# Performance work log

Hardware: AMD Instinct MI355X
Metric: run time of the kernel (lower is better)

The kernel has to match this reference:

```python
import jax, jax.numpy as jnp
import numpy as np
import math

B, L, D, H, DEPTH = 2, 1024, 1024, 16, 4
INNER = int(D * 4 * 2 / 3)  # 2730
HD = D // H
SCALE = D ** 0.5


def _get_slopes(n):
    def pow2(n):
        start = 2 ** (-2 ** (-(math.log2(n) - 3)))
        return [start * start ** i for i in range(n)]
    if math.log2(n).is_integer():
        return pow2(n)
    c = 2 ** math.floor(math.log2(n))
    return pow2(c) + _get_slopes(2 * c)[0::2][: n - c]


def setup_inputs() -> dict:
    key = jax.random.key(0)
    ks = jax.random.split(key, 8)
    def rn(k, shape, s=0.02):
        return jax.random.normal(k, shape, dtype=jnp.float32) * s
    return {
        "x": jax.random.normal(ks[0], (B, L, D), dtype=jnp.float32),
        "slopes": jnp.asarray(np.asarray(_get_slopes(H), dtype=np.float32).reshape(H, 1, 1)),
        "gamma_attn": jnp.ones((DEPTH, D), jnp.float32),
        "in_proj_w": rn(ks[1], (DEPTH, 3 * D, D)),
        "in_proj_b": jnp.zeros((DEPTH, 3 * D), jnp.float32),
        "out_proj_w": rn(ks[2], (DEPTH, D, D)),
        "out_proj_b": jnp.zeros((DEPTH, D), jnp.float32),
        "gamma_ff": jnp.ones((DEPTH, D), jnp.float32),
        "ff_w1": rn(ks[3], (DEPTH, 2 * INNER, D)),
        "ff_b1": jnp.zeros((DEPTH, 2 * INNER), jnp.float32),
        "ff_w2": rn(ks[4], (DEPTH, D, INNER)),
        "ff_b2": jnp.zeros((DEPTH, D), jnp.float32),
        "final_gamma": jnp.ones((D,), jnp.float32),
    }


def _rmsnorm(t, gamma):
    # F.normalize(x, dim=-1) * sqrt(dim) * gamma
    n = jnp.linalg.norm(t, axis=-1, keepdims=True)
    return t / jnp.maximum(n, 1e-12) * SCALE * gamma


def reference(x, slopes, gamma_attn, in_proj_w, in_proj_b, out_proj_w, out_proj_b,
              gamma_ff, ff_w1, ff_b1, ff_w2, ff_b2, final_gamma):
    Bsz, Ls, Dm = x.shape
    pos = jnp.arange(Ls)
    # ALiBi bias: -(|i-j|) * per-head slope -> (H, L, L); shared across batch
    alibi = (-jnp.abs(pos[None, :] - pos[:, None]).astype(jnp.float32))[None] * slopes
    for i in range(DEPTH):
        # attention block
        a_in = _rmsnorm(x, gamma_attn[i])
        qkv = a_in @ in_proj_w[i].T + in_proj_b[i]  # (B, L, 3D)
        q, k, v = jnp.split(qkv, 3, axis=-1)
        q = q.reshape(Bsz, Ls, H, HD).transpose(0, 2, 1, 3)
        k = k.reshape(Bsz, Ls, H, HD).transpose(0, 2, 1, 3)
        v = v.reshape(Bsz, Ls, H, HD).transpose(0, 2, 1, 3)
        scores = jnp.einsum('bhqd,bhkd->bhqk', q, k) / math.sqrt(HD) + alibi[None]
        attn = jax.nn.softmax(scores, axis=-1)
        o = jnp.einsum('bhqk,bhkd->bhqd', attn, v).transpose(0, 2, 1, 3).reshape(Bsz, Ls, Dm)
        x = o @ out_proj_w[i].T + out_proj_b[i] + x
        # GEGLU feed-forward block
        f_in = _rmsnorm(x, gamma_ff[i])
        h = f_in @ ff_w1[i].T + ff_b1[i]
        a, gate = jnp.split(h, 2, axis=-1)
        x = (jax.nn.gelu(gate, approximate=False) * a) @ ff_w2[i].T + ff_b2[i] + x
    return _rmsnorm(x, final_gamma)
```

## Files before the change

### kernel.cpp

```cpp
#include <hip/hip_runtime.h>

#define DEPTH   4
#define BSZ     2
#define LSEQ    1024
#define DMODEL  1024
#define NHEAD   16
#define HDIM    64
#define MROWS   (BSZ*LSEQ)
#define INNER   2730
#define INNERP  2752
#define N1      (2*INNER)
#define N1P     (2*INNERP)
#define LOG2E   1.4426950408889634f
#define NSPLIT  2

typedef __bf16 bf16;
typedef bf16  bf16x8 __attribute__((ext_vector_type(8)));
typedef float f32x4  __attribute__((ext_vector_type(4)));
typedef uint32_t u32x4 __attribute__((ext_vector_type(4)));

__device__ inline f32x4 mfma16(bf16x8 a, bf16x8 b, f32x4 c) {
  return __builtin_amdgcn_mfma_f32_16x16x32_bf16(a, b, c, 0, 0, 0);
}

__device__ inline void gload_lds16(const void* g, void* l) {
  __builtin_amdgcn_global_load_lds(
      (const __attribute__((address_space(1))) void*)g,
      (__attribute__((address_space(3))) void*)l, 16, 0, 0);
}

__global__ void conv_bf16_kernel(const float* __restrict__ src, bf16* __restrict__ dst, size_t n) {
  size_t i = ((size_t)blockIdx.x * 256 + threadIdx.x) * 8;
  if (i >= n) return;
  float4 v0 = *(const float4*)(src + i);
  float4 v1 = *(const float4*)(src + i + 4);
  bf16x8 o = { (bf16)v0.x,(bf16)v0.y,(bf16)v0.z,(bf16)v0.w,
               (bf16)v1.x,(bf16)v1.y,(bf16)v1.z,(bf16)v1.w };
  *(bf16x8*)(dst + i) = o;
}

__global__ void conv_w1_kernel(const float* __restrict__ src, bf16* __restrict__ dst) {
  size_t i = ((size_t)blockIdx.x * 256 + threadIdx.x) * 8;
  const size_t tot = (size_t)DEPTH * N1P * DMODEL;
  if (i >= tot) return;
  int d  = (int)(i / ((size_t)N1P * DMODEL));
  int rem = (int)(i % ((size_t)N1P * DMODEL));
  int rp = rem / DMODEL, k = rem % DMODEL;
  int p2 = rp >> 4, w = rp & 15;
  int col = ((p2 >> 1) << 4) + w;
  bf16x8 o;
  if (col >= INNER) {
    o = (bf16x8)(bf16)0.f;
  } else {
    int rs = (p2 & 1) ? (INNER + col) : col;
    const float* s = src + ((size_t)d * N1 + rs) * DMODEL + k;
    float4 v0 = *(const float4*)s;
    float4 v1 = *(const float4*)(s + 4);
    o = bf16x8{ (bf16)v0.x,(bf16)v0.y,(bf16)v0.z,(bf16)v0.w,
                (bf16)v1.x,(bf16)v1.y,(bf16)v1.z,(bf16)v1.w };
  }
  *(bf16x8*)(dst + i) = o;
}

__global__ void conv_b1_kernel(const float* __restrict__ src, float* __restrict__ dst) {
  int i = blockIdx.x * 256 + threadIdx.x;
  if (i >= DEPTH * N1P) return;
  int d = i / N1P, rp = i % N1P;
  int p2 = rp >> 4, w = rp & 15;
  int col = ((p2 >> 1) << 4) + w;
  float v = 0.f;
  if (col < INNER) v = src[d * N1 + ((p2 & 1) ? (INNER + col) : col)];
  dst[i] = v;
}

__global__ void conv_w2_kernel(const float* __restrict__ src, bf16* __restrict__ dst) {
  size_t i = ((size_t)blockIdx.x * 256 + threadIdx.x) * 8;
  const size_t tot = (size_t)DEPTH * DMODEL * INNERP;
  if (i >= tot) return;
  size_t dn = i / INNERP;
  int kp = (int)(i % INNERP);
  const float* s = src + dn * INNER;
  bf16x8 o;
  #pragma unroll
  for (int j = 0; j < 8; ++j) {
    int k = kp + j;
    o[j] = (k < INNER) ? (bf16)s[k] : (bf16)0.f;
  }
  *(bf16x8*)(dst + i) = o;
}

template<bool OUT_BF16>
__global__ __launch_bounds__(256) void rmsnorm_kernel(const float* __restrict__ x,
    const float* __restrict__ gamma, void* __restrict__ out) {
  const int row = blockIdx.x;
  const int tid = threadIdx.x;
  const float4 v = *(const float4*)(x + (size_t)row * DMODEL + tid * 4);
  float ss = v.x*v.x + v.y*v.y + v.z*v.z + v.w*v.w;
  for (int m = 1; m < 64; m <<= 1) ss += __shfl_xor(ss, m);
  __shared__ float ws4[4];
  if ((tid & 63) == 0) ws4[tid >> 6] = ss;
  __syncthreads();
  float tot = ws4[0] + ws4[1] + ws4[2] + ws4[3];
  float scale = 32.0f / fmaxf(sqrtf(tot), 1e-12f);
  const float4 g = *(const float4*)(gamma + tid * 4);
  float o0 = v.x*scale*g.x, o1 = v.y*scale*g.y, o2 = v.z*scale*g.z, o3 = v.w*scale*g.w;
  size_t p = (size_t)row * DMODEL + tid * 4;
  if (OUT_BF16) {
    bf16* ob = (bf16*)out;
    ob[p+0] = (bf16)o0; ob[p+1] = (bf16)o1; ob[p+2] = (bf16)o2; ob[p+3] = (bf16)o3;
  } else {
    *(float4*)((float*)out + p) = make_float4(o0, o1, o2, o3);
  }
}

template<int TN, int EPI, bool CHUNK_M>
__global__ __launch_bounds__(256) void gemm_bt(const bf16* __restrict__ A,
    const bf16* __restrict__ Bw, const float* __restrict__ bias,
    void* __restrict__ Cout, int M_, int N_, int Kstr, int nk0, int nkTot) {
  constexpr int NFR = TN / 32;
  constexpr int BCH = TN / 32;
  __shared__ __attribute__((aligned(16))) bf16 As[2][128 * 64];
  __shared__ __attribute__((aligned(16))) bf16 Bs[2][TN * 64];
  const int tid  = threadIdx.x;
  const int lane = tid & 63;
  const int wid  = tid >> 6;
  const int wr = wid >> 1, wc = wid & 1;

  const int z = blockIdx.z;
  const int nk  = z ? (nkTot - nk0) : nk0;
  const int kOff = z * (nk0 << 6);

  const int gx = gridDim.x, gy = gridDim.y;
  const int nwg = gx * gy;
  int bid = blockIdx.y * gx + blockIdx.x;
  int swz = bid;
  if ((nwg & 7) == 0) swz = (bid & 7) * (nwg >> 3) + (bid >> 3);
  int mIdx, nIdx;
  if (CHUNK_M) { nIdx = swz % gx; mIdx = swz / gx; }
  else         { mIdx = swz % gy; nIdx = swz / gy; }
  const int m0 = mIdx * 128;
  const int n0 = nIdx * TN;

  const int q = lane & 15, G = lane >> 4;
  const int s7 = q & 7;
  const int srow = tid >> 3;
  const int scol = ((tid & 7) ^ (srow & 7)) << 3;

  f32x4 acc[4][NFR] = {};

  auto stage = [&](int buf, int kt) {
    const int k0 = kOff + (kt << 6);
    #pragma unroll
    for (int j = 0; j < 4; ++j) {
      gload_lds16(A + (size_t)(m0 + j*32 + srow) * Kstr + k0 + scol,
                  &As[buf][(j * 256 + wid * 64) << 3]);
    }
    #pragma unroll
    for (int j = 0; j < BCH; ++j) {
      gload_lds16(Bw + (size_t)(n0 + j*32 + srow) * Kstr + k0 + scol,
                  &Bs[buf][(j * 256 + wid * 64) << 3]);
    }
  };

  stage(0, 0);
  asm volatile("s_waitcnt vmcnt(0)" ::: "memory");
  __syncthreads();

  int cur = 0;
  for (int kt = 0; kt < nk; ++kt) {
    if (kt + 1 < nk) stage(cur ^ 1, kt + 1);
    #pragma unroll
    for (int kk = 0; kk < 2; ++kk) {
      const int c0 = kk * 4 + G;
      bf16x8 af[4], bfr[NFR];
      #pragma unroll
      for (int m = 0; m < 4; ++m)
        af[m] = *(const bf16x8*)(&As[cur][(wr*64 + m*16 + q) * 64 + ((c0 ^ s7) << 3)]);
      #pragma unroll
      for (int n = 0; n < NFR; ++n)
        bfr[n] = *(const bf16x8*)(&Bs[cur][(wc*(TN/2) + n*16 + q) * 64 + ((c0 ^ s7) << 3)]);
      #pragma unroll
      for (int m = 0; m < 4; ++m)
        #pragma unroll
        for (int n = 0; n < NFR; ++n)
          acc[m][n] = mfma16(af[m], bfr[n], acc[m][n]);
    }
    asm volatile("s_waitcnt vmcnt(0)" ::: "memory");
    __syncthreads();
    cur ^= 1;
  }

  const int rb = G << 2;
  const int cl = q;
  if (EPI == 2) {
    #pragma unroll
    for (int m = 0; m < 4; ++m) {
      #pragma unroll
      for (int np = 0; np < NFR/2; ++np) {
        int ca = n0 + wc*(TN/2) + (2*np)*16 + cl;
        int cg = ca + 16;
        float ba = bias[ca], bg = bias[cg];
        int colo = ((ca >> 5) << 4) + cl;
        #pragma unroll
        for (int r = 0; r < 4; ++r) {
          int row = m0 + wr*64 + m*16 + rb + r;
          float av = acc[m][2*np][r] + ba;
          float gv = acc[m][2*np+1][r] + bg;
          float gl = 0.5f * gv * (1.f + erff(gv * 0.70710678118654752f));
          ((bf16*)Cout)[(size_t)row * (N_ >> 1) + colo] = (bf16)(av * gl);
        }
      }
    }
  } else if (EPI == 3) {
    #pragma unroll
    for (int m = 0; m < 4; ++m) {
      #pragma unroll
      for (int n = 0; n < NFR; ++n) {
        int col = n0 + wc*(TN/2) + n*16 + cl;
        float bv = (z == 0) ? bias[col] : 0.f;
        #pragma unroll
        for (int r = 0; r < 4; ++r) {
          int row = m0 + wr*64 + m*16 + rb + r;
          atomicAdd((float*)Cout + (size_t)row * N_ + col, acc[m][n][r] + bv);
        }
      }
    }
  } else {
    #pragma unroll
    for (int m = 0; m < 4; ++m) {
      #pragma unroll
      for (int n = 0; n < NFR; ++n) {
        int col = n0 + wc*(TN/2) + n*16 + cl;
        float bv = bias[col];
        #pragma unroll
        for (int r = 0; r < 4; ++r) {
          int row = m0 + wr*64 + m*16 + rb + r;
          ((bf16*)Cout)[(size_t)row * N_ + col] = (bf16)(acc[m][n][r] + bv);
        }
      }
    }
  }
}

__global__ __launch_bounds__(256) void attn_kernel(const bf16* __restrict__ qkv,
    const float* __restrict__ slopes, float* __restrict__ Opart, float* __restrict__ ml) {
  const int tid = threadIdx.x, lane = tid & 63, wid = tid >> 6;
  const int bh = blockIdx.y;
  const int b = bh >> 4, h = bh & 15;
  const int kvz = blockIdx.z;
  const int kv0 = kvz * (LSEQ / NSPLIT);
  const float slope2 = slopes[h] * LOG2E;
  const float SC = 0.125f * LOG2E;
  const int qw = blockIdx.x * 64 + wid * 16;

  __shared__ __attribute__((aligned(16))) bf16     Kt[64 * 72];
  __shared__ __attribute__((aligned(16))) uint32_t V32[64 * 36];
  __shared__ __attribute__((aligned(16))) uint32_t Pl32[4][16 * 36];

  const size_t rs = 3 * DMODEL;
  const size_t base = (size_t)b * LSEQ * rs;

  bf16x8 qf[2];
  {
    const bf16* p = qkv + base + (size_t)(qw + (lane & 15)) * rs + h * HDIM + ((lane >> 4) << 3);
    qf[0] = *(const bf16x8*)p;
    qf[1] = *(const bf16x8*)(p + 32);
  }

  f32x4 accO[4] = {};
  float mrow[4], lrow[4];
  #pragma unroll
  for (int r = 0; r < 4; ++r) { mrow[r] = -1e30f; lrow[r] = 0.f; }

  const int trow = tid >> 2;
  const int tcol = (tid & 3) << 4;

  bf16x8 kreg0, kreg1, vreg0, vreg1;
  {
    const bf16* kp = qkv + base + (size_t)(kv0 + trow) * rs + DMODEL + h * HDIM + tcol;
    kreg0 = *(const bf16x8*)kp; kreg1 = *(const bf16x8*)(kp + 8);
    const bf16* vp = qkv + base + (size_t)(kv0 + trow) * rs + 2 * DMODEL + h * HDIM + tcol;
    vreg0 = *(const bf16x8*)vp; vreg1 = *(const bf16x8*)(vp + 8);
  }

  uint32_t* P32w = &Pl32[wid][0];
  const int q = lane & 15, G = lane >> 4;

  for (int kv = kv0; kv < kv0 + LSEQ / NSPLIT; kv += 64) {
    __syncthreads();
    *(bf16x8*)(Kt + trow * 72 + tcol)     = kreg0;
    *(bf16x8*)(Kt + trow * 72 + tcol + 8) = kreg1;
    {
      u32x4 va = __builtin_bit_cast(u32x4, vreg0);
      u32x4 vb = __builtin_bit_cast(u32x4, vreg1);
      u32x4 pa, pb;
      #pragma unroll
      for (int i = 0; i < 4; ++i) {
        pa[i] = (uint32_t)__shfl_xor((int)va[i], 4);
        pb[i] = (uint32_t)__shfl_xor((int)vb[i], 4);
      }
      const bool oddk = (trow & 1);
      const int d0 = tcol + (oddk ? 8 : 0);
      u32x4 m = oddk ? vb : va;
      u32x4 oo = oddk ? pb : pa;
      const int kpair = trow >> 1;
      const int swz = kpair ^ ((d0 >> 3) << 1);
      #pragma unroll
      for (int i = 0; i < 4; ++i) {
        uint32_t lo = oddk ? oo[i] : m[i];
        uint32_t hi = oddk ? m[i] : oo[i];
        uint32_t w0 = (lo & 0xffffu) | (hi << 16);
        uint32_t w1 = (lo >> 16) | (hi & 0xffff0000u);
        V32[(d0 + 2*i)     * 36 + swz] = w0;
        V32[(d0 + 2*i + 1) * 36 + swz] = w1;
      }
    }
    __syncthreads();

    if (kv + 64 < kv0 + LSEQ / NSPLIT) {
      const bf16* kp = qkv + base + (size_t)(kv + 64 + trow) * rs + DMODEL + h * HDIM + tcol;
      kreg0 = *(const bf16x8*)kp; kreg1 = *(const bf16x8*)(kp + 8);
      const bf16* vp = qkv + base + (size_t)(kv + 64 + trow) * rs + 2 * DMODEL + h * HDIM + tcol;
      vreg0 = *(const bf16x8*)vp; vreg1 = *(const bf16x8*)(vp + 8);
    }

    f32x4 sacc[4] = {};
    __builtin_amdgcn_s_setprio(1);
    #pragma unroll
    for (int nt = 0; nt < 4; ++nt) {
      const bf16* kb = Kt + (nt * 16 + q) * 72 + (G << 3);
      sacc[nt] = mfma16(qf[0], *(const bf16x8*)kb, sacc[nt]);
      sacc[nt] = mfma16(qf[1], *(const bf16x8*)(kb + 32), sacc[nt]);
    }
    __builtin_amdgcn_s_setprio(0);

    float pv[4][4];
    #pragma unroll
    for (int r = 0; r < 4; ++r) {
      int qi = qw + (G << 2) + r;
      float vmax = -1e30f;
      #pragma unroll
      for (int nt = 0; nt < 4; ++nt) {
        int kj = kv + nt * 16 + q;
        float s = sacc[nt][r] * SC - slope2 * fabsf((float)(qi - kj));
        pv[nt][r] = s;
        vmax = fmaxf(vmax, s);
      }
      for (int m = 1; m < 16; m <<= 1) vmax = fmaxf(vmax, __shfl_xor(vmax, m));
      float newmax = fmaxf(mrow[r], vmax);
      float ef = exp2f(mrow[r] - newmax);
      float rsum = 0.f;
      #pragma unroll
      for (int nt = 0; nt < 4; ++nt) {
        float p = exp2f(pv[nt][r] - newmax);
        pv[nt][r] = p;
        rsum += p;
      }
      for (int m = 1; m < 16; m <<= 1) rsum += __shfl_xor(rsum, m);
      lrow[r] = lrow[r] * ef + rsum;
      mrow[r] = newmax;
      #pragma unroll
      for (int dn = 0; dn < 4; ++dn) accO[dn][r] *= ef;
    }

    #pragma unroll
    for (int nt = 0; nt < 4; ++nt) {
      #pragma unroll
      for (int r = 0; r < 4; ++r) {
        float other = __shfl_xor(pv[nt][r], 1);
        if (!(lane & 1)) {
          uint32_t w;
          asm("v_cvt_pk_bf16_f32 %0, %1, %2" : "=v"(w) : "v"(pv[nt][r]), "v"(other));
          int prow = (G << 2) + r;
          int col2 = nt * 8 + (q >> 1);
          P32w[prow * 36 + (col2 ^ ((prow & 7) << 1))] = w;
        }
      }
    }
    asm volatile("s_waitcnt lgkmcnt(0)" ::: "memory");

    __builtin_amdgcn_s_setprio(1);
    #pragma unroll
    for (int chunk = 0; chunk < 2; ++chunk) {
      u32x4 praw = *(const u32x4*)(P32w + q * 36 + chunk * 16 + 4 * (G ^ ((q >> 1) & 3)));
      if (q & 1) praw = __builtin_shufflevector(praw, praw, 2, 3, 0, 1);
      bf16x8 pf = __builtin_bit_cast(bf16x8, praw);
      #pragma unroll
      for (int dn = 0; dn < 4; ++dn) {
        const int d = dn * 16 + q;
        u32x4 raw = *(const u32x4*)(V32 + d * 36 + chunk * 16 + 4 * (G ^ dn));
        if ((lane >> 3) & 1) raw = __builtin_shufflevector(raw, raw, 2, 3, 0, 1);
        bf16x8 vf = __builtin_bit_cast(bf16x8, raw);
        accO[dn] = mfma16(pf, vf, accO[dn]);
      }
    }
    __builtin_amdgcn_s_setprio(0);
  }

  #pragma unroll
  for (int r = 0; r < 4; ++r) {
    int qr = qw + (G << 2) + r;
    size_t obase = ((size_t)(kvz * 32 + bh) * LSEQ + qr) * HDIM;
    #pragma unroll
    for (int dn = 0; dn < 4; ++dn)
      Opart[obase + dn * 16 + q] = accO[dn][r];
    if (q == 0) {
      size_t mb = ((size_t)(kvz * 32 + bh) * LSEQ + qr) * 2;
      ml[mb]     = mrow[r];
      ml[mb + 1] = lrow[r];
    }
  }
}

__global__ __launch_bounds__(256) void attn_combine(const float* __restrict__ Opart,
    const float* __restrict__ ml, bf16* __restrict__ o) {
  int idx = blockIdx.x * 256 + threadIdx.x;
  int bh = idx >> 14;
  int rem = idx & 16383;
  int qr = rem >> 4;
  int d4 = (rem & 15) << 2;
  float mz[NSPLIT], lz[NSPLIT];
  float m = -1e30f;
  #pragma unroll
  for (int z = 0; z < NSPLIT; ++z) {
    size_t rz = ((size_t)(z * 32 + bh) * LSEQ + qr) * 2;
    mz[z] = ml[rz]; lz[z] = ml[rz + 1];
    m = fmaxf(m, mz[z]);
  }
  float wz[NSPLIT];
  float l = 0.f;
  #pragma unroll
  for (int z = 0; z < NSPLIT; ++z) { wz[z] = exp2f(mz[z] - m); l += lz[z] * wz[z]; }
  float inv = 1.f / l;
  float ax = 0, ay = 0, az = 0, aw = 0;
  #pragma unroll
  for (int z = 0; z < NSPLIT; ++z) {
    size_t rz = (size_t)(z * 32 + bh) * LSEQ + qr;
    float4 ov = *(const float4*)(Opart + rz * HDIM + d4);
    ax += ov.x * wz[z]; ay += ov.y * wz[z]; az += ov.z * wz[z]; aw += ov.w * wz[z];
  }
  int b = bh >> 4, h = bh & 15;
  bf16* op = o + ((size_t)(b * LSEQ + qr) * DMODEL + h * HDIM + d4);
  op[0] = (bf16)(ax * inv);
  op[1] = (bf16)(ay * inv);
  op[2] = (bf16)(az * inv);
  op[3] = (bf16)(aw * inv);
}

extern "C" void kernel_launch(void* const* d_in, const int* in_sizes, int n_in,
                              void* d_out, int out_size, void* d_ws, size_t ws_size,
                              hipStream_t stream) {
  const float* x_in      = (const float*)d_in[0];
  const float* slopes    = (const float*)d_in[1];
  const float* g_attn    = (const float*)d_in[2];
  const float* w_in      = (const float*)d_in[3];
  const float* b_in      = (const float*)d_in[4];
  const float* w_out     = (const float*)d_in[5];
  const float* b_out     = (const float*)d_in[6];
  const float* g_ff      = (const float*)d_in[7];
  const float* w1        = (const float*)d_in[8];
  const float* b1        = (const float*)d_in[9];
  const float* w2        = (const float*)d_in[10];
  const float* b2        = (const float*)d_in[11];
  const float* g_final   = (const float*)d_in[12];

  char* p = (char*)d_ws;
  float* xw   = (float*)p;              p += (size_t)MROWS * DMODEL * 4;
  bf16* abuf  = (bf16*)p;               p += (size_t)MROWS * DMODEL * 2;
  bf16* qkvb  = (bf16*)p;               p += (size_t)MROWS * 3 * DMODEL * 2;
  bf16* obuf  = (bf16*)p;               p += (size_t)MROWS * DMODEL * 2;
  bf16* gbuf  = (bf16*)p;               p += (size_t)MROWS * INNERP * 2;
  float* Opart = (float*)p;             p += (size_t)NSPLIT * 32 * LSEQ * HDIM * 4;
  float* mlb   = (float*)p;             p += (size_t)NSPLIT * 32 * LSEQ * 2 * 4;
  bf16* w_in_b  = (bf16*)p;             p += (size_t)DEPTH * 3 * DMODEL * DMODEL * 2;
  bf16* w_out_b = (bf16*)p;             p += (size_t)DEPTH * DMODEL * DMODEL * 2;
  bf16* w1p     = (bf16*)p;             p += (size_t)DEPTH * N1P * DMODEL * 2;
  bf16* w2p     = (bf16*)p;             p += (size_t)DEPTH * DMODEL * INNERP * 2;
  float* b1p    = (float*)p;            p += (size_t)DEPTH * N1P * 4;

  hipMemcpyAsync(xw, x_in, (size_t)MROWS * DMODEL * 4, hipMemcpyDeviceToDevice, stream);

  conv_bf16_kernel<<<6144, 256, 0, stream>>>(w_in, w_in_b, (size_t)DEPTH * 3 * DMODEL * DMODEL);
  conv_bf16_kernel<<<2048, 256, 0, stream>>>(w_out, w_out_b, (size_t)DEPTH * DMODEL * DMODEL);
  conv_w1_kernel<<<11008, 256, 0, stream>>>(w1, w1p);
  conv_b1_kernel<<<86, 256, 0, stream>>>(b1, b1p);
  conv_w2_kernel<<<5504, 256, 0, stream>>>(w2, w2p);

  for (int i = 0; i < DEPTH; ++i) {
    rmsnorm_kernel<true><<<MROWS, 256, 0, stream>>>(xw, g_attn + i * DMODEL, abuf);
    gemm_bt<64, 0, false><<<dim3(48, 16), 256, 0, stream>>>(
        abuf, w_in_b + (size_t)i * 3 * DMODEL * DMODEL, b_in + i * 3 * DMODEL,
        qkvb, MROWS, 3 * DMODEL, DMODEL, 16, 16);
    attn_kernel<<<dim3(16, 32, NSPLIT), 256, 0, stream>>>(qkvb, slopes, Opart, mlb);
    attn_combine<<<2048, 256, 0, stream>>>(Opart, mlb, obuf);
    gemm_bt<64, 3, true><<<dim3(16, 16, 2), 256, 0, stream>>>(
        obuf, w_out_b + (size_t)i * DMODEL * DMODEL, b_out + i * DMODEL,
        xw, MROWS, DMODEL, DMODEL, 8, 16);
    rmsnorm_kernel<true><<<MROWS, 256, 0, stream>>>(xw, g_ff + i * DMODEL, abuf);
    gemm_bt<64, 2, false><<<dim3(86, 16), 256, 0, stream>>>(
        abuf, w1p + (size_t)i * N1P * DMODEL, b1p + i * N1P,
        gbuf, MROWS, N1P, DMODEL, 16, 16);
    gemm_bt<64, 3, true><<<dim3(16, 16, 2), 256, 0, stream>>>(
        gbuf, w2p + (size_t)i * DMODEL * INNERP, b2 + i * DMODEL,
        xw, MROWS, DMODEL, INNERP, 22, 43);
  }
  rmsnorm_kernel<false><<<MROWS, 256, 0, stream>>>(xw, g_final, d_out);
}
```

Measured before the change: 794.5 us.

## Transpose QK^T MFMA in attention to keep softmax rows lane-local, skip LDS for P

```diff
diff --git a/kernel.cpp b/kernel.cpp
--- a/kernel.cpp
+++ b/kernel.cpp
@@ -255,22 +255,21 @@
 
   __shared__ __attribute__((aligned(16))) bf16     Kt[64 * 72];
   __shared__ __attribute__((aligned(16))) uint32_t V32[64 * 36];
-  __shared__ __attribute__((aligned(16))) uint32_t Pl32[4][16 * 36];
 
   const size_t rs = 3 * DMODEL;
   const size_t base = (size_t)b * LSEQ * rs;
+  const int q = lane & 15, G = lane >> 4;
+  const float qi = (float)(qw + q);
 
   bf16x8 qf[2];
   {
-    const bf16* p = qkv + base + (size_t)(qw + (lane & 15)) * rs + h * HDIM + ((lane >> 4) << 3);
+    const bf16* p = qkv + base + (size_t)(qw + q) * rs + h * HDIM + (G << 3);
     qf[0] = *(const bf16x8*)p;
     qf[1] = *(const bf16x8*)(p + 32);
   }
 
   f32x4 accO[4] = {};
-  float mrow[4], lrow[4];
-  #pragma unroll
-  for (int r = 0; r < 4; ++r) { mrow[r] = -1e30f; lrow[r] = 0.f; }
+  float mreg = -1e30f, lreg = 0.f;
 
   const int trow = tid >> 2;
   const int tcol = (tid & 3) << 4;
@@ -282,9 +281,6 @@
     const bf16* vp = qkv + base + (size_t)(kv0 + trow) * rs + 2 * DMODEL + h * HDIM + tcol;
     vreg0 = *(const bf16x8*)vp; vreg1 = *(const bf16x8*)(vp + 8);
   }
-
-  uint32_t* P32w = &Pl32[wid][0];
-  const int q = lane & 15, G = lane >> 4;
 
   for (int kv = kv0; kv < kv0 + LSEQ / NSPLIT; kv += 64) {
     __syncthreads();
@@ -329,62 +325,75 @@
     #pragma unroll
     for (int nt = 0; nt < 4; ++nt) {
       const bf16* kb = Kt + (nt * 16 + q) * 72 + (G << 3);
-      sacc[nt] = mfma16(qf[0], *(const bf16x8*)kb, sacc[nt]);
-      sacc[nt] = mfma16(qf[1], *(const bf16x8*)(kb + 32), sacc[nt]);
+      sacc[nt] = mfma16(*(const bf16x8*)kb, qf[0], sacc[nt]);
+      sacc[nt] = mfma16(*(const bf16x8*)(kb + 32), qf[1], sacc[nt]);
     }
     __builtin_amdgcn_s_setprio(0);
 
     float pv[4][4];
-    #pragma unroll
-    for (int r = 0; r < 4; ++r) {
-      int qi = qw + (G << 2) + r;
-      float vmax = -1e30f;
-      #pragma unroll
-      for (int nt = 0; nt < 4; ++nt) {
-        int kj = kv + nt * 16 + q;
-        float s = sacc[nt][r] * SC - slope2 * fabsf((float)(qi - kj));
+    float pmax = -1e30f;
+    #pragma unroll
+    for (int nt = 0; nt < 4; ++nt) {
+      #pragma unroll
+      for (int r = 0; r < 4; ++r) {
+        float kj = (float)(kv + nt * 16 + (G << 2) + r);
+        float s = sacc[nt][r] * SC - slope2 * fabsf(qi - kj);
         pv[nt][r] = s;
-        vmax = fmaxf(vmax, s);
-      }
-      for (int m = 1; m < 16; m <<= 1) vmax = fmaxf(vmax, __shfl_xor(vmax, m));
-      float newmax = fmaxf(mrow[r], vmax);
-      float ef = exp2f(mrow[r] - newmax);
-      float rsum = 0.f;
-      #pragma unroll
-      for (int nt = 0; nt < 4; ++nt) {
-        float p = exp2f(pv[nt][r] - newmax);
-        pv[nt][r] = p;
-        rsum += p;
-      }
-      for (int m = 1; m < 16; m <<= 1) rsum += __shfl_xor(rsum, m);
-      lrow[r] = lrow[r] * ef + rsum;
-      mrow[r] = newmax;
-      #pragma unroll
-      for (int dn = 0; dn < 4; ++dn) accO[dn][r] *= ef;
-    }
-
+        pmax = fmaxf(pmax, s);
+      }
+    }
+    pmax = fmaxf(pmax, __shfl_xor(pmax, 16));
+    pmax = fmaxf(pmax, __shfl_xor(pmax, 32));
+
+    if (!__all(pmax <= mreg + 8.f)) {
+      float mnew = fmaxf(mreg, pmax);
+      float ef = exp2f(mreg - mnew);
+      mreg = mnew;
+      lreg *= ef;
+      float efr[4];
+      #pragma unroll
+      for (int r = 0; r < 4; ++r)
+        efr[r] = __shfl(ef, (G << 4) + (G << 2) + r);
+      #pragma unroll
+      for (int dn = 0; dn < 4; ++dn)
+        #pragma unroll
+        for (int r = 0; r < 4; ++r)
+          accO[dn][r] *= efr[r];
+    }
+
+    float rsum = 0.f;
     #pragma unroll
     for (int nt = 0; nt < 4; ++nt) {
       #pragma unroll
       for (int r = 0; r < 4; ++r) {
-        float other = __shfl_xor(pv[nt][r], 1);
-        if (!(lane & 1)) {
-          uint32_t w;
-          asm("v_cvt_pk_bf16_f32 %0, %1, %2" : "=v"(w) : "v"(pv[nt][r]), "v"(other));
-          int prow = (G << 2) + r;
-          int col2 = nt * 8 + (q >> 1);
-          P32w[prow * 36 + (col2 ^ ((prow & 7) << 1))] = w;
-        }
-      }
-    }
-    asm volatile("s_waitcnt lgkmcnt(0)" ::: "memory");
+        float pe = exp2f(pv[nt][r] - mreg);
+        pv[nt][r] = pe;
+        rsum += pe;
+      }
+    }
+    rsum += __shfl_xor(rsum, 16);
+    rsum += __shfl_xor(rsum, 32);
+    lreg += rsum;
+
+    uint32_t wp[4][2];
+    #pragma unroll
+    for (int nt = 0; nt < 4; ++nt) {
+      asm("v_cvt_pk_bf16_f32 %0, %1, %2" : "=v"(wp[nt][0]) : "v"(pv[nt][0]), "v"(pv[nt][1]));
+      asm("v_cvt_pk_bf16_f32 %0, %1, %2" : "=v"(wp[nt][1]) : "v"(pv[nt][2]), "v"(pv[nt][3]));
+    }
 
     __builtin_amdgcn_s_setprio(1);
     #pragma unroll
     for (int chunk = 0; chunk < 2; ++chunk) {
-      u32x4 praw = *(const u32x4*)(P32w + q * 36 + chunk * 16 + 4 * (G ^ ((q >> 1) & 3)));
-      if (q & 1) praw = __builtin_shufflevector(praw, praw, 2, 3, 0, 1);
-      bf16x8 pf = __builtin_bit_cast(bf16x8, praw);
+      u32x4 u;
+      #pragma unroll
+      for (int j = 0; j < 4; ++j) {
+        int src = (((G & 1) * 2 + (j >> 1)) << 4) | q;
+        uint32_t lo2 = (uint32_t)__shfl((int)wp[2*chunk][j & 1], src);
+        uint32_t hi2 = (uint32_t)__shfl((int)wp[2*chunk + 1][j & 1], src);
+        u[j] = (G & 2) ? hi2 : lo2;
+      }
+      bf16x8 pf = __builtin_bit_cast(bf16x8, u);
       #pragma unroll
       for (int dn = 0; dn < 4; ++dn) {
         const int d = dn * 16 + q;
@@ -404,11 +413,11 @@
     #pragma unroll
     for (int dn = 0; dn < 4; ++dn)
       Opart[obase + dn * 16 + q] = accO[dn][r];
-    if (q == 0) {
-      size_t mb = ((size_t)(kvz * 32 + bh) * LSEQ + qr) * 2;
-      ml[mb]     = mrow[r];
-      ml[mb + 1] = lrow[r];
-    }
+  }
+  if (lane < 16) {
+    size_t mb = ((size_t)(kvz * 32 + bh) * LSEQ + qw + lane) * 2;
+    ml[mb]     = mreg;
+    ml[mb + 1] = lreg;
   }
 }
 
```

Result: faster. 701.0 us (-11.8%).
